# Kernel optimization log

Hardware: AMD Instinct MI355X
Metric: run time of the kernel (lower is better)

## Reference

```python
import jax, jax.numpy as jnp
import numpy as np

N_HEADS = 16
DIM = 1024
DPH = DIM // N_HEADS  # 64
NEG_INF = -1e20       # neginf(float32) in the torch source


def setup_inputs() -> dict:
    key0 = jax.random.key(0)
    ks = jax.random.split(key0, 12)
    bs, qlen, nrev, klen = 32, 128, 20, 64
    w = lambda k: jax.random.normal(k, (DIM, DIM), jnp.float32) * 0.02
    return {
        "query": jax.random.normal(ks[0], (bs, qlen, DIM), jnp.float32),
        "key": jax.random.normal(ks[1], (bs, nrev, klen, DIM), jnp.float32),
        "value": jax.random.normal(ks[2], (bs, nrev, klen, DIM), jnp.float32),
        "mask": jax.random.randint(ks[3], (bs, nrev), 0, 2, jnp.int32),
        "mask2": jax.random.randint(ks[4], (bs, nrev, klen), 0, 2, jnp.int32),
        "Wq": w(ks[5]), "bq": jnp.zeros((DIM,), jnp.float32),
        "Wk": w(ks[6]), "bk": jnp.zeros((DIM,), jnp.float32),
        "Wv": w(ks[7]), "bv": jnp.zeros((DIM,), jnp.float32),
        "Wo": w(ks[8]), "bo": jnp.zeros((DIM,), jnp.float32),
        "sa_a": jax.random.normal(ks[9], (DPH, DPH), jnp.float32) * 0.1,
        "sa_b": jax.random.normal(ks[10], (DPH, 1), jnp.float32) * 0.1,
    }


def _forward(query, key, value, mask, mask2,
             Wq, bq, Wk, bk, Wv, bv, Wo, bo, sa_a, sa_b):
    bs, qlen, dim = query.shape
    _, nrev, klen, _ = key.shape
    dph = dim // N_HEADS
    scale = float(dph) ** 0.5

    # linear projections + head split (torch Linear: x @ W.T + b)
    q = (query @ Wq.T + bq).reshape(bs, qlen, N_HEADS, dph)        # [B,Q,H,d]
    k = (key @ Wk.T + bk).reshape(bs, nrev, klen, N_HEADS, dph)    # [B,R,T,H,d]
    v = (value @ Wv.T + bv).reshape(bs, nrev, klen, N_HEADS, dph)  # [B,R,T,H,d]

    # --- token-level attention: per review, q attends over review tokens ---
    scores = jnp.einsum('bqhd,brthd->bhrqt', q, k) / scale          # [B,H,R,Q,T]
    tok_pad = (mask2 == 0)[:, None, :, None, :]                     # [B,1,R,1,T]
    scores = jnp.where(tok_pad, NEG_INF, scores)
    attn_w = jax.nn.softmax(scores, axis=-1)
    att = jnp.einsum('bhrqt,brthd->bhqrd', attn_w, v)               # [B,H,Q,R,d]

    # --- review-level self-attention pooling (SelfAttentionSeq) ---
    # e = tanh(h @ a) @ b ; mask applied only if some reviews have mask==0,
    # and then NONZERO mask positions get -1e30 (faithful to the source).
    e = jnp.tanh(att @ sa_a) @ sa_b                                 # [B,H,Q,R,1]
    e = e[..., 0]                                                   # [B,H,Q,R]
    mf = mask.astype(att.dtype)                                     # [B,R]
    any_zero = (jnp.sum(mask == 0, axis=-1, keepdims=True) > 0).astype(att.dtype)  # [B,1]
    add_mask = (-1e30 * mf) * any_zero                              # [B,R]
    e = e + add_mask[:, None, None, :]
    rev_w = jax.nn.softmax(e, axis=-1)                              # [B,H,Q,R]
    pooled = jnp.einsum('bhqr,bhqrd->bhqd', rev_w, att)             # [B,H,Q,d]

    # merge heads + output projection
    merged = pooled.transpose(0, 2, 1, 3).reshape(bs, qlen, dim)    # [B,Q,D]
    return merged @ Wo.T + bo


def reference(query, key, value, mask, mask2,
              Wq, bq, Wk, bk, Wv, bv, Wo, bo, sa_a, sa_b):
    return _forward(query, key, value, mask, mask2,
                    Wq, bq, Wk, bk, Wv, bv, Wo, bo, sa_a, sa_b)
```

## Files before the change

kernel.cpp:

```cpp
#include <hip/hip_runtime.h>
#include <stdint.h>


typedef __attribute__((ext_vector_type(8))) short bf16x8;
typedef __attribute__((ext_vector_type(4))) float f32x4;
typedef __attribute__((ext_vector_type(4))) unsigned int u32x4;
typedef __attribute__((address_space(1))) const unsigned int as1_t;
typedef __attribute__((address_space(3))) unsigned int as3_t;

#define DEVI static __device__ __forceinline__

DEVI unsigned short f2bf(float f) {
  unsigned int u = __float_as_uint(f);
  u += 0x7fffu + ((u >> 16) & 1u);
  return (unsigned short)(u >> 16);
}
DEVI unsigned int pack2(float a, float b) {
  return (unsigned int)f2bf(a) | ((unsigned int)f2bf(b) << 16);
}
DEVI unsigned int cvtpk(float a, float b) {
  unsigned int r;
  asm("v_cvt_pk_bf16_f32 %0, %1, %2" : "=v"(r) : "v"(a), "v"(b));
  return r;
}

DEVI void gload_lds16(const void* g, void* l) {
  __builtin_amdgcn_global_load_lds((as1_t*)g, (as3_t*)l, 16, 0, 0);
}

DEVI float fast_tanh(float x) {
  float ax = fabsf(x);
  float e = __expf(2.0f * ax);
  float r = __builtin_fmaf(-2.0f, __builtin_amdgcn_rcpf(e + 1.0f), 1.0f);
  return copysignf(r, x);
}

DEVI void cvt_sparse_body(const float* __restrict__ src,
                          unsigned short* __restrict__ dst,
                          const unsigned char* actb, int gid, int stride) {
  for (int u = gid; u < 640 * 8192; u += stride) {
    const int s = u >> 13;
    if (!actb[s]) continue;
    f32x4 a = *(const f32x4*)(src + (size_t)u * 8);
    f32x4 b = *(const f32x4*)(src + (size_t)u * 8 + 4);
    u32x4 o = {pack2(a[0], a[1]), pack2(a[2], a[3]),
               pack2(b[0], b[1]), pack2(b[2], b[3])};
    *(u32x4*)(dst + (size_t)u * 8) = o;
  }
}

DEVI void build_actb(const int* __restrict__ mask, unsigned char* actb,
                     int* azs, int tid) {
  if (tid < 32) {
    int z = 0;
#pragma unroll
    for (int r = 0; r < 20; ++r) z |= (mask[tid * 20 + r] == 0) ? 1 : 0;
    azs[tid] = z;
  }
  __syncthreads();
  for (int s = tid; s < 640; s += 256)
    actb[s] = azs[s / 20] ? ((mask[s] == 0) ? 1 : 0) : 1;
  __syncthreads();
}

__global__ __launch_bounds__(256) void prep(
    const float* __restrict__ w0, const float* __restrict__ w1,
    const float* __restrict__ w2, const float* __restrict__ w3,
    unsigned short* __restrict__ o0, unsigned short* __restrict__ o1,
    unsigned short* __restrict__ o2, unsigned short* __restrict__ o3,
    const float* __restrict__ qsrc, unsigned short* __restrict__ qdst,
    const float* __restrict__ ksrc, unsigned short* __restrict__ kdst,
    const int* __restrict__ mask, int* __restrict__ cmp) {
  const int bx = (int)blockIdx.x;
  const int tid = (int)threadIdx.x;
  if (bx < 1024) {
    const int i = bx * 256 + tid;
    f32x4 v;
    uint2 a;
    v = ((const f32x4*)w0)[i]; a.x = pack2(v[0], v[1]); a.y = pack2(v[2], v[3]);
    *(uint2*)(o0 + 4 * (size_t)i) = a;
    v = ((const f32x4*)w1)[i]; a.x = pack2(v[0], v[1]); a.y = pack2(v[2], v[3]);
    *(uint2*)(o1 + 4 * (size_t)i) = a;
    v = ((const f32x4*)w2)[i]; a.x = pack2(v[0], v[1]); a.y = pack2(v[2], v[3]);
    *(uint2*)(o2 + 4 * (size_t)i) = a;
    v = ((const f32x4*)w3)[i]; a.x = pack2(v[0], v[1]); a.y = pack2(v[2], v[3]);
    *(uint2*)(o3 + 4 * (size_t)i) = a;
  } else if (bx < 2048) {
    const int i = (bx - 1024) * 256 + tid;
#pragma unroll
    for (int h = 0; h < 2; ++h) {
      const int u = i + h * 262144;
      f32x4 a = ((const f32x4*)qsrc)[2 * u];
      f32x4 b = ((const f32x4*)qsrc)[2 * u + 1];
      u32x4 o = {pack2(a[0], a[1]), pack2(a[2], a[3]),
                 pack2(b[0], b[1]), pack2(b[2], b[3])};
      ((u32x4*)qdst)[u] = o;
    }
  } else if (bx == 2048) {
    __shared__ int azs[32];
    if (tid < 32) {
      int z = 0;
#pragma unroll
      for (int r = 0; r < 20; ++r) z |= (mask[tid * 20 + r] == 0) ? 1 : 0;
      azs[tid] = z;
    }
    __syncthreads();
    if (tid < 64) {
      const int lane = tid;
      int base = 0;
      int lasts = 0;
      for (int it = 0; it < 10; ++it) {
        const int s = it * 64 + lane;
        const int bb = s / 20;
        const int actv = azs[bb] ? ((mask[s] == 0) ? 1 : 0) : 1;
        unsigned long long bal = __ballot(actv);
        const int off = (int)__popcll(bal & ((1ull << lane) - 1ull));
        if (actv) {
          cmp[1 + base + off] = s;
          lasts = s;
        }
        base += (int)__popcll(bal);
      }
#pragma unroll
      for (int d = 1; d < 64; d <<= 1) {
        int o = __shfl_xor(lasts, d);
        lasts = lasts > o ? lasts : o;
      }
      if (lane == 0) {
        cmp[0] = base;
        cmp[1 + base] = lasts;
      }
    }
  } else {
    __shared__ unsigned char actb[640];
    __shared__ int azs[32];
    build_actb(mask, actb, azs, tid);
    cvt_sparse_body(ksrc, kdst, actb, (bx - 2049) * 256 + tid, 2048 * 256);
  }
}

__global__ __launch_bounds__(256) void cvt_sp(const float* __restrict__ src,
                                              unsigned short* __restrict__ dst,
                                              const int* __restrict__ mask) {
  __shared__ unsigned char actb[640];
  __shared__ int azs[32];
  const int tid = (int)threadIdx.x;
  build_actb(mask, actb, azs, tid);
  cvt_sparse_body(src, dst, actb, (int)(blockIdx.x * 256) + tid,
                  (int)(gridDim.x * 256));
}

template <int OUT_MODE, int SC, int CMP>
DEVI void gemm_body(const void* __restrict__ Ain,
                    const unsigned short* __restrict__ W,
                    const float* __restrict__ bias, void* __restrict__ Cout,
                    int N, int K, int nnt, int nb, int bx,
                    const int* __restrict__ cmp, char* smem) {
  char* Asb = smem;
  char* Bsb = smem + 16384;
  const int tid = (int)threadIdx.x;
  const int lane = tid & 63, wave = tid >> 6;
  const int lm = lane & 15, l4 = lane >> 4;
  const int wr = wave >> 1, wc = wave & 1;

  int mt, nt, cs0, cs1;
  if (CMP) {
    const int cnt = cmp[0];
    const int tiles = (cnt + 1) >> 1;
    if (bx >= tiles * 8) return;
    const int lg = (bx & 7) * tiles + (bx >> 3);
    mt = lg / nnt;
    nt = lg % nnt;
    cs0 = cmp[1 + 2 * mt];
    cs1 = cmp[2 + 2 * mt];
  } else {
    const int lg = (bx & 7) * (nb >> 3) + (bx >> 3);
    mt = lg / nnt;
    nt = lg % nnt;
    cs0 = 2 * mt;
    cs1 = 2 * mt + 1;
  }

  f32x4 zero4 = {0.f, 0.f, 0.f, 0.f};
  f32x4 acc[4][4];
#pragma unroll
  for (int i = 0; i < 4; ++i)
#pragma unroll
    for (int j = 0; j < 4; ++j) acc[i][j] = zero4;

  const int srow = tid >> 2, sblk = tid & 3;
  const int scb = sblk ^ ((srow >> 1) & 3);
  const unsigned short* wpg = W + (size_t)(nt * 128 + srow) * K + scb * 8;
  const int kx = (lm >> 1) & 3;

  const unsigned short* apg0 =
      (const unsigned short*)Ain + ((size_t)cs0 * 64 + srow) * K + scb * 8;
  const unsigned short* apg1 =
      (const unsigned short*)Ain + ((size_t)cs1 * 64 + srow) * K + scb * 8;
  const int NT = K >> 5;
#pragma unroll
  for (int t0 = 0; t0 < 2; ++t0) {
    const int kt = t0 * 32;
    gload_lds16(apg0 + kt, Asb + t0 * 8192 + tid * 16);
    gload_lds16(apg1 + kt, Asb + t0 * 8192 + 4096 + tid * 16);
    gload_lds16(wpg + kt, Bsb + t0 * 8192 + tid * 16);
    gload_lds16(wpg + (size_t)64 * K + kt, Bsb + t0 * 8192 + 4096 + tid * 16);
  }
  int cur = 0;
  for (int t = 0; t < NT; ++t) {
    if (t + 1 < NT)
      asm volatile("s_waitcnt vmcnt(4)" ::: "memory");
    else
      asm volatile("s_waitcnt vmcnt(0)" ::: "memory");
    asm volatile("s_barrier" ::: "memory");
    bf16x8 af[4], bfr[4];
#pragma unroll
    for (int i = 0; i < 4; ++i)
      af[i] = *(const bf16x8*)(Asb + cur * 8192 + (wr * 64 + i * 16 + lm) * 64 +
                               ((l4 ^ kx) * 16));
#pragma unroll
    for (int j = 0; j < 4; ++j)
      bfr[j] = *(const bf16x8*)(Bsb + cur * 8192 + (wc * 64 + j * 16 + lm) * 64 +
                                ((l4 ^ kx) * 16));
#pragma unroll
    for (int i = 0; i < 4; ++i)
#pragma unroll
      for (int j = 0; j < 4; ++j)
        acc[i][j] = __builtin_amdgcn_mfma_f32_16x16x32_bf16(af[i], bfr[j], acc[i][j], 0, 0, 0);
    asm volatile("s_barrier" ::: "memory");
    if (t + 2 < NT) {
      const int kt = (t + 2) * 32;
      gload_lds16(apg0 + kt, Asb + cur * 8192 + tid * 16);
      gload_lds16(apg1 + kt, Asb + cur * 8192 + 4096 + tid * 16);
      gload_lds16(wpg + kt, Bsb + cur * 8192 + tid * 16);
      gload_lds16(wpg + (size_t)64 * K + kt, Bsb + cur * 8192 + 4096 + tid * 16);
    }
    cur ^= 1;
  }

  const int c0o = nt * 128 + wc * 64 + lm;
  float bb[4];
#pragma unroll
  for (int j = 0; j < 4; ++j) bb[j] = bias[c0o + j * 16];
  const int mslot = wr ? cs1 : cs0;

  if (OUT_MODE < 2) {
#pragma unroll
    for (int i = 0; i < 4; ++i)
#pragma unroll
      for (int j = 0; j < 4; ++j)
#pragma unroll
        for (int p = 0; p < 4; ++p) {
          size_t grow = (size_t)mslot * 64 + (l4 * 4 + i * 16 + p);
          size_t idx = grow * N + (size_t)(c0o + j * 16);
          float v = acc[i][j][p] + bb[j];
          if (SC) v *= 0.125f;
          if (OUT_MODE == 1)
            ((unsigned short*)Cout)[idx] = f2bf(v);
          else
            ((float*)Cout)[idx] = v;
        }
  } else {
    const int hh = (nt * 128 + wc * 64) / 64;
    unsigned short* vt = (unsigned short*)Cout;
    const size_t base = ((size_t)mslot * 16 + hh) * 4096;
#pragma unroll
    for (int j = 0; j < 4; ++j) {
      const int d = lm + j * 16;
#pragma unroll
      for (int i = 0; i < 4; ++i) {
        uint2 wv;
        wv.x = pack2(acc[i][j][0] + bb[j], acc[i][j][1] + bb[j]);
        wv.y = pack2(acc[i][j][2] + bb[j], acc[i][j][3] + bb[j]);
        *(uint2*)(vt + base + (size_t)d * 64 + i * 16 + l4 * 4) = wv;
      }
    }
  }
}

__global__ __launch_bounds__(256, 4) void gemm_qk(
    const unsigned short* __restrict__ aq, const unsigned short* __restrict__ wq,
    const float* __restrict__ bq, unsigned short* __restrict__ qout,
    const unsigned short* __restrict__ ak, const unsigned short* __restrict__ wk,
    const float* __restrict__ bk, unsigned short* __restrict__ kout,
    const int* __restrict__ cmp) {
  __shared__ __align__(16) char smem[32768];
  const int bx = (int)blockIdx.x;
  if (bx < 256)
    gemm_body<1, 1, 0>(aq, wq, bq, qout, 1024, 1024, 8, 256, bx, cmp, smem);
  else
    gemm_body<1, 0, 1>(ak, wk, bk, kout, 1024, 1024, 8, 2560, bx - 256, cmp, smem);
}

__global__ __launch_bounds__(256, 4) void gemm_qkv(
    const unsigned short* __restrict__ aq, const unsigned short* __restrict__ wq,
    const float* __restrict__ bq, unsigned short* __restrict__ qout,
    const unsigned short* __restrict__ ak, const unsigned short* __restrict__ wk,
    const float* __restrict__ bk, unsigned short* __restrict__ kout,
    const float* __restrict__ vsrc, unsigned short* __restrict__ vdst,
    const int* __restrict__ mask, const int* __restrict__ cmp) {
  __shared__ __align__(16) char smem[32768];
  const int bx = (int)blockIdx.x;
  const int tid = (int)threadIdx.x;
  if (bx < 256) {
    gemm_body<1, 1, 0>(aq, wq, bq, qout, 1024, 1024, 8, 256, bx, cmp, smem);
  } else if (bx < 256 + 2560) {
    gemm_body<1, 0, 1>(ak, wk, bk, kout, 1024, 1024, 8, 2560, bx - 256, cmp, smem);
  } else {
    unsigned char* actb = (unsigned char*)smem;
    int* azs = (int*)(smem + 640);
    build_actb(mask, actb, azs, tid);
    cvt_sparse_body(vsrc, vdst, actb, (bx - 2816) * 256 + tid, 2048 * 256);
  }
}

__global__ __launch_bounds__(256, 4) void gemm_v(
    const unsigned short* __restrict__ av, const unsigned short* __restrict__ wv,
    const float* __restrict__ bv, unsigned short* __restrict__ vout,
    const int* __restrict__ cmp) {
  __shared__ __align__(16) char smem[32768];
  gemm_body<2, 0, 1>(av, wv, bv, vout, 1024, 1024, 8, 2560, (int)blockIdx.x, cmp, smem);
}

__global__ __launch_bounds__(256, 4) void gemm_out(
    const unsigned short* __restrict__ am, const unsigned short* __restrict__ wo,
    const float* __restrict__ bo, float* __restrict__ oout,
    const int* __restrict__ cmp) {
  __shared__ __align__(16) char smem[32768];
  gemm_body<0, 0, 0>(am, wo, bo, oout, 1024, 1024, 8, 256, (int)blockIdx.x, cmp, smem);
}

__global__ __launch_bounds__(512, 4) void attn2(
    const unsigned short* __restrict__ qb, const unsigned short* __restrict__ kb,
    const unsigned short* __restrict__ vtg, const int* __restrict__ mask,
    const int* __restrict__ mask2, const float* __restrict__ sa_a,
    const float* __restrict__ sa_b, unsigned short* __restrict__ merged) {
  const int h = (int)blockIdx.x;
  const int b = (int)blockIdx.y;
  const int tid = (int)threadIdx.x;
  const int lane = tid & 63, wave = tid >> 6;
  const int lm = lane & 15, l4 = lane >> 4;
  const int sw = (lm & 7) << 4;

  __shared__ unsigned short kv_s[2][2][64 * 64];
  __shared__ unsigned short pa_s[8 * 16 * 64];

  char* kvb0 = (char*)kv_s;
  char* qreg = (char*)kv_s + 16384;
  char* satb = (char*)pa_s;

  unsigned am = 0u;
#pragma unroll
  for (int rr = 0; rr < 20; ++rr)
    am |= (mask[b * 20 + rr] == 0) ? (1u << rr) : 0u;
  const unsigned act = am ? am : 0xFFFFFu;

#pragma unroll
  for (int s = 0; s < 2; ++s) {
    int idx = s * 512 + tid, row = idx >> 3, blk = idx & 7;
    int cb = blk ^ (row & 7);
    gload_lds16(qb + (size_t)(b * 128 + row) * 1024 + h * 64 + cb * 8, qreg + idx * 16);
  }
#pragma unroll
  for (int s = 0; s < 8; ++s) {
    int idx = s * 512 + tid, jj = idx & 63, d = idx >> 6;
    *(unsigned short*)(satb + jj * 128 + ((d * 2) ^ ((jj & 7) << 4))) =
        f2bf(sa_a[d * 64 + jj]);
  }
  const int srow = tid >> 3, sblk = tid & 7;
  const int scb = sblk ^ (srow & 7);
  int r = (int)__builtin_ctz(act);
  unsigned rem = act & (act - 1u);
  gload_lds16(kb + ((size_t)(b * 20 + r) * 64 + srow) * 1024 + h * 64 + scb * 8,
              kvb0 + tid * 16);
  gload_lds16(vtg + ((size_t)(b * 20 + r) * 16 + h) * 4096 + srow * 64 + scb * 8,
              kvb0 + 8192 + tid * 16);

  f32x4 sbv[4];
#pragma unroll
  for (int i = 0; i < 4; ++i) sbv[i] = *(const f32x4*)(sa_b + i * 16 + l4 * 4);

  __syncthreads();

  const char* qrp = qreg + (wave * 16 + lm) * 128;
  bf16x8 qf[2];
  qf[0] = *(const bf16x8*)(qrp + ((l4 * 16) ^ sw));
  qf[1] = *(const bf16x8*)(qrp + ((64 + l4 * 16) ^ sw));
  bf16x8 sfr[2][4];
#pragma unroll
  for (int kk = 0; kk < 2; ++kk)
#pragma unroll
    for (int i = 0; i < 4; ++i)
      sfr[kk][i] = *(const bf16x8*)(satb + (i * 16 + lm) * 128 +
                                    ((kk * 64 + l4 * 16) ^ sw));
  asm volatile("s_waitcnt lgkmcnt(0)" ::: "memory");
  __syncthreads();

  char* pw = (char*)pa_s + wave * 2048 + lm * 128;

  f32x4 zero4 = {0.f, 0.f, 0.f, 0.f};
  f32x4 Pacc[4];
#pragma unroll
  for (int i = 0; i < 4; ++i) Pacc[i] = zero4;
  float m_run = -3.0e38f, s_run = 0.0f;

  int it = 0;
  for (;;) {
    const int pb = it & 1;
    if (it) __syncthreads();
    const int nr = rem ? (int)__builtin_ctz(rem) : -1;
    if (nr >= 0) {
      const int nbuf = pb ^ 1;
      gload_lds16(kb + ((size_t)(b * 20 + nr) * 64 + srow) * 1024 + h * 64 + scb * 8,
                  kvb0 + nbuf * 16384 + tid * 16);
      gload_lds16(vtg + ((size_t)(b * 20 + nr) * 16 + h) * 4096 + srow * 64 + scb * 8,
                  kvb0 + nbuf * 16384 + 8192 + tid * 16);
    }
    const char* kbse = kvb0 + pb * 16384;
    const char* vbse = kvb0 + pb * 16384 + 8192;

    const int mbase = (b * 20 + r) * 64;
    int4 m2v[4];
#pragma unroll
    for (int i = 0; i < 4; ++i)
      m2v[i] = *(const int4*)(mask2 + mbase + i * 16 + l4 * 4);

    f32x4 sc[4];
#pragma unroll
    for (int i = 0; i < 4; ++i) sc[i] = zero4;
    __builtin_amdgcn_s_setprio(1);
#pragma unroll
    for (int kk = 0; kk < 2; ++kk) {
      bf16x8 kf[4];
#pragma unroll
      for (int i = 0; i < 4; ++i)
        kf[i] = *(const bf16x8*)(kbse + (i * 16 + lm) * 128 + ((kk * 64 + l4 * 16) ^ sw));
#pragma unroll
      for (int i = 0; i < 4; ++i)
        sc[i] = __builtin_amdgcn_mfma_f32_16x16x32_bf16(kf[i], qf[kk], sc[i], 0, 0, 0);
    }
    __builtin_amdgcn_s_setprio(0);

#pragma unroll
    for (int i = 0; i < 4; ++i) {
      sc[i][0] = (m2v[i].x == 0) ? -1e20f : sc[i][0];
      sc[i][1] = (m2v[i].y == 0) ? -1e20f : sc[i][1];
      sc[i][2] = (m2v[i].z == 0) ? -1e20f : sc[i][2];
      sc[i][3] = (m2v[i].w == 0) ? -1e20f : sc[i][3];
    }
    float mx = sc[0][0];
#pragma unroll
    for (int i = 0; i < 4; ++i)
#pragma unroll
      for (int p = 0; p < 4; ++p) mx = fmaxf(mx, sc[i][p]);
    mx = fmaxf(mx, __shfl_xor(mx, 16));
    mx = fmaxf(mx, __shfl_xor(mx, 32));
    float sum = 0.f;
#pragma unroll
    for (int i = 0; i < 4; ++i)
#pragma unroll
      for (int p = 0; p < 4; ++p) {
        float e = __expf(sc[i][p] - mx);
        sc[i][p] = e;
        sum += e;
      }
    sum += __shfl_xor(sum, 16);
    sum += __shfl_xor(sum, 32);
    const float pinv = __builtin_amdgcn_rcpf(sum);

#pragma unroll
    for (int i = 0; i < 4; ++i) {
      uint2 wv;
      wv.x = cvtpk(sc[i][0] * pinv, sc[i][1] * pinv);
      wv.y = cvtpk(sc[i][2] * pinv, sc[i][3] * pinv);
      *(uint2*)(pw + ((i * 32 + l4 * 8) ^ sw)) = wv;
    }

    f32x4 av[4];
#pragma unroll
    for (int i = 0; i < 4; ++i) av[i] = zero4;
    __builtin_amdgcn_s_setprio(1);
#pragma unroll
    for (int kk = 0; kk < 2; ++kk) {
      bf16x8 pf = *(const bf16x8*)(pw + ((kk * 64 + l4 * 16) ^ sw));
      bf16x8 vf[4];
#pragma unroll
      for (int i = 0; i < 4; ++i)
        vf[i] = *(const bf16x8*)(vbse + (i * 16 + lm) * 128 + ((kk * 64 + l4 * 16) ^ sw));
#pragma unroll
      for (int i = 0; i < 4; ++i)
        av[i] = __builtin_amdgcn_mfma_f32_16x16x32_bf16(vf[i], pf, av[i], 0, 0, 0);
    }
    __builtin_amdgcn_s_setprio(0);

#pragma unroll
    for (int i = 0; i < 4; ++i) {
      uint2 wv;
      wv.x = cvtpk(av[i][0], av[i][1]);
      wv.y = cvtpk(av[i][2], av[i][3]);
      *(uint2*)(pw + ((i * 32 + l4 * 8) ^ sw)) = wv;
    }

    f32x4 ep[4];
#pragma unroll
    for (int i = 0; i < 4; ++i) ep[i] = zero4;
    __builtin_amdgcn_s_setprio(1);
#pragma unroll
    for (int kk = 0; kk < 2; ++kk) {
      bf16x8 afr = *(const bf16x8*)(pw + ((kk * 64 + l4 * 16) ^ sw));
#pragma unroll
      for (int i = 0; i < 4; ++i)
        ep[i] = __builtin_amdgcn_mfma_f32_16x16x32_bf16(sfr[kk][i], afr, ep[i], 0, 0, 0);
    }
    __builtin_amdgcn_s_setprio(0);
    float a = 0.f;
#pragma unroll
    for (int i = 0; i < 4; ++i)
#pragma unroll
      for (int p = 0; p < 4; ++p) a += fast_tanh(ep[i][p]) * sbv[i][p];
    a += __shfl_xor(a, 16);
    a += __shfl_xor(a, 32);

    const float e_r = a;
    const float mnew = fmaxf(m_run, e_r);
    const float scl = __expf(m_run - mnew);
    const float w = __expf(e_r - mnew);
    s_run = s_run * scl + w;
#pragma unroll
    for (int i = 0; i < 4; ++i)
#pragma unroll
      for (int p = 0; p < 4; ++p) Pacc[i][p] = Pacc[i][p] * scl + w * av[i][p];
    m_run = mnew;

    if (nr < 0) break;
    r = nr;
    rem &= rem - 1u;
    ++it;
  }

  const float inv_s = __builtin_amdgcn_rcpf(s_run);
  unsigned short* mrow = merged + (size_t)(b * 128 + wave * 16 + lm) * 1024 + h * 64;
#pragma unroll
  for (int i = 0; i < 4; ++i) {
    uint2 o;
    o.x = cvtpk(Pacc[i][0] * inv_s, Pacc[i][1] * inv_s);
    o.y = cvtpk(Pacc[i][2] * inv_s, Pacc[i][3] * inv_s);
    *(uint2*)(mrow + i * 16 + l4 * 4) = o;
  }
}

extern "C" void kernel_launch(void* const* d_in, const int* in_sizes, int n_in,
                              void* d_out, int out_size, void* d_ws, size_t ws_size,
                              hipStream_t stream) {
  (void)in_sizes; (void)n_in; (void)out_size;
  const float* query = (const float*)d_in[0];
  const float* key   = (const float*)d_in[1];
  const float* value = (const float*)d_in[2];
  const int*   mask  = (const int*)d_in[3];
  const int*   mask2 = (const int*)d_in[4];
  const float* Wq = (const float*)d_in[5];
  const float* bq = (const float*)d_in[6];
  const float* Wk = (const float*)d_in[7];
  const float* bk = (const float*)d_in[8];
  const float* Wv = (const float*)d_in[9];
  const float* bv = (const float*)d_in[10];
  const float* Wo = (const float*)d_in[11];
  const float* bo = (const float*)d_in[12];
  const float* sa_a = (const float*)d_in[13];
  const float* sa_b = (const float*)d_in[14];

  char* ws = (char*)d_ws;
  size_t off = 0;
  auto carve = [&](size_t bytes) -> char* {
    char* p = ws + off;
    off += (bytes + 255) & ~(size_t)255;
    return p;
  };
  unsigned short* wq_b = (unsigned short*)carve((size_t)1024 * 1024 * 2);
  unsigned short* wk_b = (unsigned short*)carve((size_t)1024 * 1024 * 2);
  unsigned short* wv_b = (unsigned short*)carve((size_t)1024 * 1024 * 2);
  unsigned short* wo_b = (unsigned short*)carve((size_t)1024 * 1024 * 2);
  unsigned short* q_b  = (unsigned short*)carve((size_t)4096 * 1024 * 2);
  unsigned short* k_b  = (unsigned short*)carve((size_t)40960 * 1024 * 2);
  unsigned short* vt_g = (unsigned short*)carve((size_t)40960 * 1024 * 2);
  unsigned short* mrg  = (unsigned short*)carve((size_t)4096 * 1024 * 2);
  int* cmp = (int*)carve(4096);
  unsigned short* act = (unsigned short*)carve((size_t)40960 * 1024 * 2);
  unsigned short* act_q = (unsigned short*)carve((size_t)4096 * 1024 * 2);

  const size_t actv_bytes = (size_t)40960 * 1024 * 2;
  const bool fat = ws_size >= off + actv_bytes + (1 << 20);

  prep<<<4097, 256, 0, stream>>>(Wq, Wk, Wv, Wo, wq_b, wk_b, wv_b, wo_b,
                                 query, act_q, key, act, mask, cmp);

  if (fat) {
    unsigned short* act_v = (unsigned short*)carve(actv_bytes);
    gemm_qkv<<<256 + 2560 + 2048, 256, 0, stream>>>(
        act_q, wq_b, bq, q_b, act, wk_b, bk, k_b, value, act_v, mask, cmp);
    gemm_v<<<2560, 256, 0, stream>>>(act_v, wv_b, bv, vt_g, cmp);
  } else {
    gemm_qk<<<256 + 2560, 256, 0, stream>>>(act_q, wq_b, bq, q_b,
                                            act, wk_b, bk, k_b, cmp);
    cvt_sp<<<2048, 256, 0, stream>>>(value, act, mask);
    gemm_v<<<2560, 256, 0, stream>>>(act, wv_b, bv, vt_g, cmp);
  }

  attn2<<<dim3(16, 32), 512, 0, stream>>>(q_b, k_b, vt_g, mask, mask2, sa_a, sa_b, mrg);

  gemm_out<<<256, 256, 0, stream>>>(mrg, wo_b, bo, (float*)d_out, cmp);
}
```

Baseline: 253.6 us.

## Move V conversion into prep and fuse Q/K/V GEMMs into one launch

The sparse fp32-to-bf16 conversion of value now runs inside the prep kernel, which grows by 2048 blocks. The Q, K and V projection GEMMs then run together in a single kernel, so there is one fewer launch and no serial V GEMM tail. This rebalances work across kernels: prep gets longer, and the fused GEMM launch becomes larger and uniform, which should fill the GPU better. V conversion no longer overlaps with the Q/K GEMM, since it now runs before it in prep.

```diff
diff --git a/kernel.cpp b/kernel.cpp
--- a/kernel.cpp
+++ b/kernel.cpp
@@ -70,6 +70,7 @@
     unsigned short* __restrict__ o2, unsigned short* __restrict__ o3,
     const float* __restrict__ qsrc, unsigned short* __restrict__ qdst,
     const float* __restrict__ ksrc, unsigned short* __restrict__ kdst,
+    const float* __restrict__ vsrc, unsigned short* __restrict__ vdst,
     const int* __restrict__ mask, int* __restrict__ cmp) {
   const int bx = (int)blockIdx.x;
   const int tid = (int)threadIdx.x;
@@ -131,11 +132,16 @@
         cmp[1 + base] = lasts;
       }
     }
+  } else if (bx < 4097) {
+    __shared__ unsigned char actb[640];
+    __shared__ int azs[32];
+    build_actb(mask, actb, azs, tid);
+    cvt_sparse_body(ksrc, kdst, actb, (bx - 2049) * 256 + tid, 2048 * 256);
   } else {
     __shared__ unsigned char actb[640];
     __shared__ int azs[32];
     build_actb(mask, actb, azs, tid);
-    cvt_sparse_body(ksrc, kdst, actb, (bx - 2049) * 256 + tid, 2048 * 256);
+    cvt_sparse_body(vsrc, vdst, actb, (bx - 4097) * 256 + tid, 2048 * 256);
   }
 }
 
@@ -292,26 +298,22 @@
     gemm_body<1, 0, 1>(ak, wk, bk, kout, 1024, 1024, 8, 2560, bx - 256, cmp, smem);
 }
 
-__global__ __launch_bounds__(256, 4) void gemm_qkv(
+__global__ __launch_bounds__(256, 4) void gemm_qkv3(
     const unsigned short* __restrict__ aq, const unsigned short* __restrict__ wq,
     const float* __restrict__ bq, unsigned short* __restrict__ qout,
     const unsigned short* __restrict__ ak, const unsigned short* __restrict__ wk,
     const float* __restrict__ bk, unsigned short* __restrict__ kout,
-    const float* __restrict__ vsrc, unsigned short* __restrict__ vdst,
-    const int* __restrict__ mask, const int* __restrict__ cmp) {
+    const unsigned short* __restrict__ av, const unsigned short* __restrict__ wv,
+    const float* __restrict__ bv, unsigned short* __restrict__ vout,
+    const int* __restrict__ cmp) {
   __shared__ __align__(16) char smem[32768];
   const int bx = (int)blockIdx.x;
-  const int tid = (int)threadIdx.x;
-  if (bx < 256) {
+  if (bx < 256)
     gemm_body<1, 1, 0>(aq, wq, bq, qout, 1024, 1024, 8, 256, bx, cmp, smem);
-  } else if (bx < 256 + 2560) {
+  else if (bx < 256 + 2560)
     gemm_body<1, 0, 1>(ak, wk, bk, kout, 1024, 1024, 8, 2560, bx - 256, cmp, smem);
-  } else {
-    unsigned char* actb = (unsigned char*)smem;
-    int* azs = (int*)(smem + 640);
-    build_actb(mask, actb, azs, tid);
-    cvt_sparse_body(vsrc, vdst, actb, (bx - 2816) * 256 + tid, 2048 * 256);
-  }
+  else
+    gemm_body<2, 0, 1>(av, wv, bv, vout, 1024, 1024, 8, 2560, bx - 2816, cmp, smem);
 }
 
 __global__ __launch_bounds__(256, 4) void gemm_v(
@@ -591,15 +593,18 @@
   const size_t actv_bytes = (size_t)40960 * 1024 * 2;
   const bool fat = ws_size >= off + actv_bytes + (1 << 20);
 
-  prep<<<4097, 256, 0, stream>>>(Wq, Wk, Wv, Wo, wq_b, wk_b, wv_b, wo_b,
-                                 query, act_q, key, act, mask, cmp);
-
   if (fat) {
     unsigned short* act_v = (unsigned short*)carve(actv_bytes);
-    gemm_qkv<<<256 + 2560 + 2048, 256, 0, stream>>>(
-        act_q, wq_b, bq, q_b, act, wk_b, bk, k_b, value, act_v, mask, cmp);
-    gemm_v<<<2560, 256, 0, stream>>>(act_v, wv_b, bv, vt_g, cmp);
+    prep<<<6145, 256, 0, stream>>>(Wq, Wk, Wv, Wo, wq_b, wk_b, wv_b, wo_b,
+                                   query, act_q, key, act, value, act_v,
+                                   mask, cmp);
+    gemm_qkv3<<<256 + 2560 + 2560, 256, 0, stream>>>(
+        act_q, wq_b, bq, q_b, act, wk_b, bk, k_b,
+        act_v, wv_b, bv, vt_g, cmp);
   } else {
+    prep<<<4097, 256, 0, stream>>>(Wq, Wk, Wv, Wo, wq_b, wk_b, wv_b, wo_b,
+                                   query, act_q, key, act, value, act,
+                                   mask, cmp);
     gemm_qk<<<256 + 2560, 256, 0, stream>>>(act_q, wq_b, bq, q_b,
                                             act, wk_b, bk, k_b, cmp);
     cvt_sp<<<2048, 256, 0, stream>>>(value, act, mask);
```

Result: no change. 254.6 us (+0.4%).
